# Performance work log

Hardware: AMD Instinct MI355X
Metric: run time of the kernel (lower is better)

## Reference

```python
import jax, jax.numpy as jnp
import numpy as np

Nc, Ns, Nt, d_h, BS = 64, 64, 64, 128, 16


def setup_inputs() -> dict:
    key = jax.random.key(0)
    k1, k2, k3, k4, k5 = jax.random.split(key, 5)
    Ac = (jax.random.uniform(k1, (Ns, Nc)) < 0.05).astype(jnp.float32)
    As = (jax.random.uniform(k2, (Ns, Ns)) < 0.05).astype(jnp.float32)
    # AA = As@As@Ac + As@Ac + Ac, then binarize (masked_fill(AA != 0, 1))
    AA = As @ As @ Ac + As @ Ac + Ac
    AA = (AA != 0).astype(jnp.float32)                 # [Ns, Nc]
    AA_mask = jnp.tile(AA, (Nt, Nt))                   # [Ns*Nt, Nc*Nt], == AA.repeat(Nt,Nt) in torch
    GCW = jax.random.normal(k3, (Ns * Nt, Nc * Nt), dtype=jnp.float32)
    GCB = jax.random.normal(k4, (Ns * Nt, d_h), dtype=jnp.float32)
    h = jax.random.normal(k5, (BS, Nc, Nt, d_h), dtype=jnp.float32)
    e = jnp.zeros((1,), jnp.float32)                   # unused in forward (kept for signature parity)
    return {"h": h, "e": e, "AA_mask": AA_mask, "GCW": GCW, "GCB": GCB}


def reference(h, e, AA_mask, GCW, GCB):
    bs = h.shape[0]
    # A = relu(AA.repeat(Nt,Nt) * GCW)  -- structured masked weight [Ns*Nt, Nc*Nt]
    A = jax.nn.relu(AA_mask * GCW)
    # h: [bs, Nc, Nt, d_h] -> [bs, Nt, Nc, d_h] -> [bs, Nt*Nc, d_h]
    x = jnp.transpose(h, (0, 2, 1, 3)).reshape(bs, Nt * Nc, d_h)
    # relu(A @ x + GCB): [bs, Ns*Nt, d_h]
    x = jax.nn.relu(jnp.einsum('ij,bjd->bid', A, x) + GCB)
    # [bs, Nt, Ns, d_h] -> [bs, Ns, Nt, d_h] (final torch reshape is a no-op)
    x = x.reshape(bs, Nt, Ns, d_h)
    x = jnp.transpose(x, (0, 2, 1, 3))
    return x
```

## Files before the change

kernel.cpp:

```cpp
#include <hip/hip_runtime.h>


#define NC 64
#define NS 64
#define NT 64
#define DH 128
#define BATCH 16
#define MDIM 4096
#define KDIM 4096
#define KPAD 4096
#define TM 128
#define TK 64
#define GBM 64
#define GBN 256
#define GBK 64

typedef __attribute__((ext_vector_type(8))) short short8;
typedef __attribute__((ext_vector_type(4))) short short4v;
typedef __attribute__((ext_vector_type(4))) float floatx4;

__device__ __forceinline__ unsigned short f2bf(float f) {
    union { float f; unsigned int i; } v; v.f = f;
    return (unsigned short)((v.i + 0x7fffu + ((v.i >> 16) & 1u)) >> 16);
}
__device__ __forceinline__ void async16(const void* g, void* l) {
    __builtin_amdgcn_global_load_lds(
        (const __attribute__((address_space(1))) void*)g,
        (__attribute__((address_space(3))) void*)l, 16, 0, 0);
}

__global__ __launch_bounds__(256)
void prep(const float* __restrict__ aam, const float* __restrict__ gcw,
          const float* __restrict__ hmat,
          unsigned short* __restrict__ Abf, unsigned short* __restrict__ XT,
          unsigned short* __restrict__ cidx, int* __restrict__ nsb)
{
    const int tid = threadIdx.x;
    if ((int)blockIdx.x < MDIM) {
        const int r  = blockIdx.x;
        const int s  = r >> 6;
        const int tt = r & 63;
        const int i  = tt * 64 + s;
        __shared__ unsigned short scidx[64];
        __shared__ int sns;
        __shared__ unsigned short srow[4096];
        if (tid < 64) {
            float v = aam[(size_t)s * KDIM + tid];
            unsigned long long m = __ballot(v != 0.f);
            int rank = __popcll(m & ((1ull << tid) - 1ull));
            if (v != 0.f) scidx[rank] = (unsigned short)tid;
            if (tid == 0) sns = (int)__popcll(m);
            if (tt == 0) {
                if (v != 0.f) cidx[s * 64 + rank] = (unsigned short)tid;
                if (tid == 0) nsb[s] = (int)__popcll(m);
            }
        }
        const float* gr = gcw + (size_t)i * KDIM;
#pragma unroll
        for (int u = 0; u < 4; ++u) {
            const int idx = u * 1024 + tid * 4;
            floatx4 wv = *(const floatx4*)(gr + idx);
            short4v p;
#pragma unroll
            for (int e = 0; e < 4; ++e) {
                float v = wv[e] > 0.f ? wv[e] : 0.f;
                p[e] = (short)f2bf(v);
            }
            *(short4v*)&srow[idx] = p;
        }
        __syncthreads();
        const int ke = sns * 64;
        for (int kk0 = tid * 8; kk0 < ke; kk0 += 2048) {
            const int c  = (int)scidx[kk0 >> 6];
            const int t0 = kk0 & 63;
            short8 p;
#pragma unroll
            for (int e = 0; e < 8; ++e)
                p[e] = (short)srow[(t0 + e) * 64 + c];
            *(short8*)(Abf + (size_t)r * KPAD + kk0) = p;
        }
    } else {
        const int blk = blockIdx.x - MDIM;
        const int b = blk >> 6;
        const int c = blk & 63;
        __shared__ unsigned short sx[64][136];
        const float* hp = hmat + (((size_t)b * NC + c) * NT) * DH;
#pragma unroll
        for (int u = 0; u < 8; ++u) {
            const int idx = u * 1024 + tid * 4;
            const int t = idx >> 7;
            const int d = idx & 127;
            floatx4 v = *(const floatx4*)(hp + idx);
            short4v p;
#pragma unroll
            for (int e = 0; e < 4; ++e) p[e] = (short)f2bf(v[e]);
            *(short4v*)&sx[t][d] = p;
        }
        __syncthreads();
        const int d  = tid >> 1;
        const int th = (tid & 1) * 32;
        unsigned short* dst = XT + ((size_t)(b * DH + d)) * KPAD + c * 64 + th;
#pragma unroll
        for (int u2 = 0; u2 < 4; ++u2) {
            short8 p;
#pragma unroll
            for (int e = 0; e < 8; ++e)
                p[e] = (short)sx[th + u2 * 8 + e][d];
            *(short8*)(dst + u2 * 8) = p;
        }
    }
}

__global__ __launch_bounds__(256, 2)
void gemm(const unsigned short* __restrict__ Abf,
          const unsigned short* __restrict__ XT,
          const unsigned short* __restrict__ cidx,
          const int* __restrict__ nsb,
          const float* __restrict__ gcb,
          float* __restrict__ out)
{
    __shared__ short lds[2][(GBM + GBN) * GBK];

    const int tid = threadIdx.x;
    const int bid = blockIdx.x;
    const int np = bid & 7;
    const int s  = bid >> 3;
    const int n0 = np * GBN;

    const int lane = tid & 63;
    const int w    = tid >> 6;
    const int wn   = w * 64;
    const int l15  = lane & 15;
    const int q    = lane >> 4;
    const int srow = lane >> 3;
    const int swz  = ((lane & 7) ^ srow) << 3;

    const int nt = nsb[s];
    const int cl = (int)cidx[s * 64 + lane];

    const unsigned short* Ab = Abf + (size_t)(s * 64) * KPAD + swz;
    const unsigned short* Xb = XT  + (size_t)n0 * KPAD + swz;

    floatx4 acc[4][4];
#pragma unroll
    for (int mi = 0; mi < 4; ++mi)
#pragma unroll
        for (int ni = 0; ni < 4; ++ni)
            acc[mi][ni] = (floatx4){0.f, 0.f, 0.f, 0.f};

    auto stage = [&](int t, int b) {
        short* dst = lds[b];
        const int c = __shfl(cl, t);
        const size_t ka = (size_t)t * GBK;
        const size_t kx = (size_t)c * GBK;
        async16(Ab + (size_t)(w * 8 + srow) * KPAD + ka,       dst + (w * 8) * GBK);
        async16(Ab + (size_t)((w + 4) * 8 + srow) * KPAD + ka, dst + ((w + 4) * 8) * GBK);
#pragma unroll
        for (int g = 0; g < 8; ++g) {
            const int rr = w * 64 + g * 8;
            async16(Xb + (size_t)(rr + srow) * KPAD + kx, dst + (GBM + rr) * GBK);
        }
    };

    auto compute = [&](int b) {
        const short* sA = lds[b];
        const short* sX = lds[b] + GBM * GBK;
#pragma unroll
        for (int h2 = 0; h2 < 2; ++h2) {
            const int co = ((h2 * 4 + q) ^ (l15 & 7)) << 3;
            short8 af[4], xf[4];
#pragma unroll
            for (int mi = 0; mi < 4; ++mi)
                af[mi] = *(const short8*)&sA[(mi * 16 + l15) * GBK + co];
#pragma unroll
            for (int ni = 0; ni < 4; ++ni)
                xf[ni] = *(const short8*)&sX[(wn + ni * 16 + l15) * GBK + co];
            __builtin_amdgcn_s_setprio(1);
#pragma unroll
            for (int mi = 0; mi < 4; ++mi)
#pragma unroll
                for (int ni = 0; ni < 4; ++ni)
                    acc[mi][ni] = __builtin_amdgcn_mfma_f32_16x16x32_bf16(
                        af[mi], xf[ni], acc[mi][ni], 0, 0, 0);
            __builtin_amdgcn_s_setprio(0);
        }
    };

    if (nt > 0) stage(0, 0);
    if (nt > 1) stage(1, 1);
    for (int t = 0; t < nt - 1; ++t) {
        asm volatile("s_waitcnt vmcnt(10)" ::: "memory");
        __builtin_amdgcn_s_barrier();
        compute(t & 1);
        __builtin_amdgcn_s_barrier();
        if (t + 2 < nt) stage(t + 2, t & 1);
    }
    if (nt > 0) {
        asm volatile("s_waitcnt vmcnt(0)" ::: "memory");
        __builtin_amdgcn_s_barrier();
        compute((nt - 1) & 1);
    }

#pragma unroll
    for (int mi = 0; mi < 4; ++mi) {
        const int tt0 = mi * 16 + q * 4;
#pragma unroll
        for (int ni = 0; ni < 4; ++ni) {
            const int n  = n0 + wn + ni * 16 + l15;
            const int bb = n >> 7;
            const int d  = n & 127;
#pragma unroll
            for (int r = 0; r < 4; ++r) {
                const int tt = tt0 + r;
                const int i  = tt * 64 + s;
                float v = acc[mi][ni][r] + gcb[(size_t)i * DH + d];
                v = v > 0.f ? v : 0.f;
                out[(((size_t)bb * NS + s) * NT + tt) * DH + d] = v;
            }
        }
    }
}

#define APAD 40
#define XPAD 20
__global__ __launch_bounds__(256, 2)
void gcn_fused(const float* __restrict__ hmat, const float* __restrict__ aam,
               const float* __restrict__ gcw, const float* __restrict__ gcb,
               float* __restrict__ out)
{
    __shared__ short sA[TM * APAD];
    __shared__ unsigned int sX[DH * XPAD];
    const int tid = threadIdx.x;
    const int bid = blockIdx.x;
    const int mp  = (bid & 7) * 4 + (bid >> 7);
    const int b   = (bid >> 3) & 15;
    const int i0  = mp * TM;
    const int lane = tid & 63;
    const int wm = ((tid >> 6) >> 1) * 64;
    const int wn = ((tid >> 6) & 1) * 64;
    const int l15 = lane & 15;
    const int q   = lane >> 4;
    floatx4 acc[4][4];
#pragma unroll
    for (int mi = 0; mi < 4; ++mi)
#pragma unroll
        for (int ni = 0; ni < 4; ++ni) acc[mi][ni] = (floatx4){0.f,0.f,0.f,0.f};
    const int ar = tid >> 2, ac = (tid & 3) << 3;
    const int kp = tid >> 4, dg = (tid & 15) << 3;
    const int wkey = (tid & 3) << 2;
    for (int k0 = 0; k0 < KDIM; k0 += 32) {
        const size_t ga0 = (size_t)(i0 + ar) * KDIM + (k0 + ac);
        const size_t ga1 = ga0 + (size_t)64 * KDIM;
        floatx4 aa0a = *(const floatx4*)(aam + ga0), aa0b = *(const floatx4*)(aam + ga0 + 4);
        floatx4 ww0a = *(const floatx4*)(gcw + ga0), ww0b = *(const floatx4*)(gcw + ga0 + 4);
        floatx4 aa1a = *(const floatx4*)(aam + ga1), aa1b = *(const floatx4*)(aam + ga1 + 4);
        floatx4 ww1a = *(const floatx4*)(gcw + ga1), ww1b = *(const floatx4*)(gcw + ga1 + 4);
        const int jj = k0 + 2 * kp, tt = jj >> 6, cc = jj & 63;
        const size_t gx0 = ((size_t)(b * NC + cc) * NT + tt) * DH + dg;
        const size_t gx1 = gx0 + (size_t)NT * DH;
        floatx4 x0a = *(const floatx4*)(hmat + gx0), x0b = *(const floatx4*)(hmat + gx0 + 4);
        floatx4 x1a = *(const floatx4*)(hmat + gx1), x1b = *(const floatx4*)(hmat + gx1 + 4);
        __syncthreads();
        short8 p0, p1;
#pragma unroll
        for (int e = 0; e < 4; ++e) {
            float v0 = aa0a[e]*ww0a[e]; v0 = v0>0.f?v0:0.f;
            float v1 = aa0b[e]*ww0b[e]; v1 = v1>0.f?v1:0.f;
            float v2 = aa1a[e]*ww1a[e]; v2 = v2>0.f?v2:0.f;
            float v3 = aa1b[e]*ww1b[e]; v3 = v3>0.f?v3:0.f;
            p0[e] = (short)f2bf(v0); p0[e+4] = (short)f2bf(v1);
            p1[e] = (short)f2bf(v2); p1[e+4] = (short)f2bf(v3);
        }
        *(short8*)&sA[ar * APAD + ac] = p0;
        *(short8*)&sA[(ar + 64) * APAD + ac] = p1;
#pragma unroll
        for (int e = 0; e < 4; ++e) {
            unsigned int pka = (unsigned int)f2bf(x0a[e]) | ((unsigned int)f2bf(x1a[e]) << 16);
            unsigned int pkb = (unsigned int)f2bf(x0b[e]) | ((unsigned int)f2bf(x1b[e]) << 16);
            sX[(dg + e) * XPAD + (kp ^ wkey)] = pka;
            sX[(dg + e + 4) * XPAD + (kp ^ wkey)] = pkb;
        }
        __syncthreads();
        short8 afrag[4], bfrag[4];
#pragma unroll
        for (int mi = 0; mi < 4; ++mi)
            afrag[mi] = *(const short8*)&sA[(wm + mi * 16 + l15) * APAD + q * 8];
#pragma unroll
        for (int ni = 0; ni < 4; ++ni) {
            const int row = wn + ni * 16 + l15;
            const int col = (q * 4) ^ (((row >> 3) & 3) << 2);
            bfrag[ni] = *(const short8*)(sX + row * XPAD + col);
        }
#pragma unroll
        for (int mi = 0; mi < 4; ++mi)
#pragma unroll
            for (int ni = 0; ni < 4; ++ni)
                acc[mi][ni] = __builtin_amdgcn_mfma_f32_16x16x32_bf16(
                    afrag[mi], bfrag[ni], acc[mi][ni], 0, 0, 0);
    }
#pragma unroll
    for (int mi = 0; mi < 4; ++mi) {
        const int ibase = i0 + wm + mi * 16 + q * 4;
#pragma unroll
        for (int ni = 0; ni < 4; ++ni) {
            const int d = wn + ni * 16 + l15;
#pragma unroll
            for (int r = 0; r < 4; ++r) {
                const int i = ibase + r;
                float v = acc[mi][ni][r] + gcb[(size_t)i * DH + d];
                v = v > 0.f ? v : 0.f;
                out[(((size_t)b * NS + (i & 63)) * NT + (i >> 6)) * DH + d] = v;
            }
        }
    }
}

extern "C" void kernel_launch(void* const* d_in, const int* in_sizes, int n_in,
                              void* d_out, int out_size, void* d_ws, size_t ws_size,
                              hipStream_t stream) {
    const float* h   = (const float*)d_in[0];
    const float* aam = (const float*)d_in[2];
    const float* gcw = (const float*)d_in[3];
    const float* gcb = (const float*)d_in[4];
    float* out = (float*)d_out;

    const size_t A_BYTES   = (size_t)MDIM * KPAD * 2;
    const size_t XT_BYTES  = (size_t)BATCH * DH * KPAD * 2;
    const size_t IDX_BYTES = 64 * 64 * 2;
    const size_t NS_BYTES  = 64 * 4;

    if (ws_size >= A_BYTES + XT_BYTES + IDX_BYTES + NS_BYTES) {
        unsigned short* Abf = (unsigned short*)d_ws;
        unsigned short* XTp = (unsigned short*)((char*)d_ws + A_BYTES);
        unsigned short* cid = (unsigned short*)((char*)d_ws + A_BYTES + XT_BYTES);
        int* nsb            = (int*)((char*)d_ws + A_BYTES + XT_BYTES + IDX_BYTES);
        prep<<<dim3(MDIM + BATCH * NT), 256, 0, stream>>>(aam, gcw, h, Abf, XTp, cid, nsb);
        gemm<<<dim3(64 * 8), 256, 0, stream>>>(Abf, XTp, cid, nsb, gcb, out);
    } else {
        gcn_fused<<<dim3((MDIM / TM) * BATCH), 256, 0, stream>>>(h, aam, gcw, gcb, out);
    }
}
```

Baseline: 229.3 us.

## Shrink GEMM N-tile to one batch, use 8 waves, and gather GCW directly

The GEMM tile shrinks from 256 to 128 columns, so each block covers a single batch. Blocks now have 512 threads in a 2x4 wave grid with 2x2 MFMA tiles per wave, and the grid doubles to 1024 blocks, which should raise occupancy and parallelism on the many CUs. The prep kernel no longer stages the whole GCW row through LDS; it reads only the needed sparse columns directly from global memory, cutting the loaded bytes to the nonzero blocks. The cost is strided, uncoalesced gathers in prep and less data reuse per block in the GEMM.

```diff
diff --git a/kernel.cpp b/kernel.cpp
--- a/kernel.cpp
+++ b/kernel.cpp
@@ -12,7 +12,7 @@
 #define TM 128
 #define TK 64
 #define GBM 64
-#define GBN 256
+#define GBN 128
 #define GBK 64
 
 typedef __attribute__((ext_vector_type(8))) short short8;
@@ -43,7 +43,6 @@
         const int i  = tt * 64 + s;
         __shared__ unsigned short scidx[64];
         __shared__ int sns;
-        __shared__ unsigned short srow[4096];
         if (tid < 64) {
             float v = aam[(size_t)s * KDIM + tid];
             unsigned long long m = __ballot(v != 0.f);
@@ -55,28 +54,19 @@
                 if (tid == 0) nsb[s] = (int)__popcll(m);
             }
         }
-        const float* gr = gcw + (size_t)i * KDIM;
-#pragma unroll
-        for (int u = 0; u < 4; ++u) {
-            const int idx = u * 1024 + tid * 4;
-            floatx4 wv = *(const floatx4*)(gr + idx);
-            short4v p;
-#pragma unroll
-            for (int e = 0; e < 4; ++e) {
-                float v = wv[e] > 0.f ? wv[e] : 0.f;
-                p[e] = (short)f2bf(v);
-            }
-            *(short4v*)&srow[idx] = p;
-        }
         __syncthreads();
         const int ke = sns * 64;
+        const float* gr = gcw + (size_t)i * KDIM;
         for (int kk0 = tid * 8; kk0 < ke; kk0 += 2048) {
             const int c  = (int)scidx[kk0 >> 6];
             const int t0 = kk0 & 63;
             short8 p;
 #pragma unroll
-            for (int e = 0; e < 8; ++e)
-                p[e] = (short)srow[(t0 + e) * 64 + c];
+            for (int e = 0; e < 8; ++e) {
+                float v = gr[(t0 + e) * 64 + c];
+                v = v > 0.f ? v : 0.f;
+                p[e] = (short)f2bf(v);
+            }
             *(short8*)(Abf + (size_t)r * KPAD + kk0) = p;
         }
     } else {
@@ -111,7 +101,7 @@
     }
 }
 
-__global__ __launch_bounds__(256, 2)
+__global__ __launch_bounds__(512, 6)
 void gemm(const unsigned short* __restrict__ Abf,
           const unsigned short* __restrict__ XT,
           const unsigned short* __restrict__ cidx,
@@ -123,13 +113,14 @@
 
     const int tid = threadIdx.x;
     const int bid = blockIdx.x;
-    const int np = bid & 7;
-    const int s  = bid >> 3;
+    const int np = bid & 15;
+    const int s  = bid >> 4;
     const int n0 = np * GBN;
 
     const int lane = tid & 63;
     const int w    = tid >> 6;
-    const int wn   = w * 64;
+    const int wm   = (w >> 2) * 32;
+    const int wn   = (w & 3) * 32;
     const int l15  = lane & 15;
     const int q    = lane >> 4;
     const int srow = lane >> 3;
@@ -141,11 +132,11 @@
     const unsigned short* Ab = Abf + (size_t)(s * 64) * KPAD + swz;
     const unsigned short* Xb = XT  + (size_t)n0 * KPAD + swz;
 
-    floatx4 acc[4][4];
-#pragma unroll
-    for (int mi = 0; mi < 4; ++mi)
-#pragma unroll
-        for (int ni = 0; ni < 4; ++ni)
+    floatx4 acc[2][2];
+#pragma unroll
+    for (int mi = 0; mi < 2; ++mi)
+#pragma unroll
+        for (int ni = 0; ni < 2; ++ni)
             acc[mi][ni] = (floatx4){0.f, 0.f, 0.f, 0.f};
 
     auto stage = [&](int t, int b) {
@@ -154,12 +145,8 @@
         const size_t ka = (size_t)t * GBK;
         const size_t kx = (size_t)c * GBK;
         async16(Ab + (size_t)(w * 8 + srow) * KPAD + ka,       dst + (w * 8) * GBK);
-        async16(Ab + (size_t)((w + 4) * 8 + srow) * KPAD + ka, dst + ((w + 4) * 8) * GBK);
-#pragma unroll
-        for (int g = 0; g < 8; ++g) {
-            const int rr = w * 64 + g * 8;
-            async16(Xb + (size_t)(rr + srow) * KPAD + kx, dst + (GBM + rr) * GBK);
-        }
+        async16(Xb + (size_t)(w * 8 + srow) * KPAD + kx,       dst + (GBM + w * 8) * GBK);
+        async16(Xb + (size_t)(64 + w * 8 + srow) * KPAD + kx,  dst + (GBM + 64 + w * 8) * GBK);
     };
 
     auto compute = [&](int b) {
@@ -168,18 +155,18 @@
 #pragma unroll
         for (int h2 = 0; h2 < 2; ++h2) {
             const int co = ((h2 * 4 + q) ^ (l15 & 7)) << 3;
-            short8 af[4], xf[4];
-#pragma unroll
-            for (int mi = 0; mi < 4; ++mi)
-                af[mi] = *(const short8*)&sA[(mi * 16 + l15) * GBK + co];
-#pragma unroll
-            for (int ni = 0; ni < 4; ++ni)
+            short8 af[2], xf[2];
+#pragma unroll
+            for (int mi = 0; mi < 2; ++mi)
+                af[mi] = *(const short8*)&sA[(wm + mi * 16 + l15) * GBK + co];
+#pragma unroll
+            for (int ni = 0; ni < 2; ++ni)
                 xf[ni] = *(const short8*)&sX[(wn + ni * 16 + l15) * GBK + co];
             __builtin_amdgcn_s_setprio(1);
 #pragma unroll
-            for (int mi = 0; mi < 4; ++mi)
-#pragma unroll
-                for (int ni = 0; ni < 4; ++ni)
+            for (int mi = 0; mi < 2; ++mi)
+#pragma unroll
+                for (int ni = 0; ni < 2; ++ni)
                     acc[mi][ni] = __builtin_amdgcn_mfma_f32_16x16x32_bf16(
                         af[mi], xf[ni], acc[mi][ni], 0, 0, 0);
             __builtin_amdgcn_s_setprio(0);
@@ -189,7 +176,7 @@
     if (nt > 0) stage(0, 0);
     if (nt > 1) stage(1, 1);
     for (int t = 0; t < nt - 1; ++t) {
-        asm volatile("s_waitcnt vmcnt(10)" ::: "memory");
+        asm volatile("s_waitcnt vmcnt(3)" ::: "memory");
         __builtin_amdgcn_s_barrier();
         compute(t & 1);
         __builtin_amdgcn_s_barrier();
@@ -202,20 +189,18 @@
     }
 
 #pragma unroll
-    for (int mi = 0; mi < 4; ++mi) {
-        const int tt0 = mi * 16 + q * 4;
-#pragma unroll
-        for (int ni = 0; ni < 4; ++ni) {
-            const int n  = n0 + wn + ni * 16 + l15;
-            const int bb = n >> 7;
-            const int d  = n & 127;
+    for (int mi = 0; mi < 2; ++mi) {
+        const int tt0 = wm + mi * 16 + q * 4;
+#pragma unroll
+        for (int ni = 0; ni < 2; ++ni) {
+            const int d = wn + ni * 16 + l15;
 #pragma unroll
             for (int r = 0; r < 4; ++r) {
                 const int tt = tt0 + r;
                 const int i  = tt * 64 + s;
                 float v = acc[mi][ni][r] + gcb[(size_t)i * DH + d];
                 v = v > 0.f ? v : 0.f;
-                out[(((size_t)bb * NS + s) * NT + tt) * DH + d] = v;
+                out[(((size_t)np * NS + s) * NT + tt) * DH + d] = v;
             }
         }
     }
@@ -335,7 +320,7 @@
         unsigned short* cid = (unsigned short*)((char*)d_ws + A_BYTES + XT_BYTES);
         int* nsb            = (int*)((char*)d_ws + A_BYTES + XT_BYTES + IDX_BYTES);
         prep<<<dim3(MDIM + BATCH * NT), 256, 0, stream>>>(aam, gcw, h, Abf, XTp, cid, nsb);
-        gemm<<<dim3(64 * 8), 256, 0, stream>>>(Abf, XTp, cid, nsb, gcb, out);
+        gemm<<<dim3(64 * 16), 512, 0, stream>>>(Abf, XTp, cid, nsb, gcb, out);
     } else {
         gcn_fused<<<dim3((MDIM / TM) * BATCH), 256, 0, stream>>>(h, aam, gcw, gcb, out);
     }
```

Result: no change. 233.5 us (+1.8%).

## Pair sparse row-blocks in GEMM to share X tiles and gather A directly

Applied to the files above, without the earlier changes.

The GEMM now handles two output row-blocks per workgroup. It uses 512 threads and an M tile of 128, and walks the union of their nonzero column-blocks. Each staged X tile is reused by both halves, and a wave's MFMA work is skipped when its half lacks that column-block. The prep kernel no longer stages full fp32 GCW rows through LDS. Each block handles four rows and gathers only the needed nonzero columns straight from global memory, and it builds the paired column index table. This trades fewer and larger GEMM blocks plus strided, uncoalesced global reads in prep for less X traffic and less wasted conversion work.

```diff
diff --git a/kernel.cpp b/kernel.cpp
--- a/kernel.cpp
+++ b/kernel.cpp
@@ -11,7 +11,7 @@
 #define KPAD 4096
 #define TM 128
 #define TK 64
-#define GBM 64
+#define GBM 128
 #define GBN 256
 #define GBK 64
 
@@ -33,54 +33,60 @@
 void prep(const float* __restrict__ aam, const float* __restrict__ gcw,
           const float* __restrict__ hmat,
           unsigned short* __restrict__ Abf, unsigned short* __restrict__ XT,
-          unsigned short* __restrict__ cidx, int* __restrict__ nsb)
+          int* __restrict__ cpair, int* __restrict__ ntp)
 {
     const int tid = threadIdx.x;
-    if ((int)blockIdx.x < MDIM) {
-        const int r  = blockIdx.x;
-        const int s  = r >> 6;
-        const int tt = r & 63;
-        const int i  = tt * 64 + s;
+    if ((int)blockIdx.x < 1024) {
+        const int blk = blockIdx.x;
+        const int s   = blk >> 4;
+        const int tt0 = (blk & 15) * 4;
         __shared__ unsigned short scidx[64];
         __shared__ int sns;
-        __shared__ unsigned short srow[4096];
         if (tid < 64) {
             float v = aam[(size_t)s * KDIM + tid];
             unsigned long long m = __ballot(v != 0.f);
             int rank = __popcll(m & ((1ull << tid) - 1ull));
             if (v != 0.f) scidx[rank] = (unsigned short)tid;
             if (tid == 0) sns = (int)__popcll(m);
-            if (tt == 0) {
-                if (v != 0.f) cidx[s * 64 + rank] = (unsigned short)tid;
-                if (tid == 0) nsb[s] = (int)__popcll(m);
+            if (tt0 == 0 && (s & 1) == 0) {
+                float v1 = aam[(size_t)(s + 1) * KDIM + tid];
+                unsigned long long m1 = __ballot(v1 != 0.f);
+                unsigned long long mu = m | m1;
+                if ((mu >> tid) & 1ull) {
+                    int ur  = __popcll(mu & ((1ull << tid) - 1ull));
+                    int ci0 = __popcll(m  & ((1ull << tid) - 1ull));
+                    int ci1 = __popcll(m1 & ((1ull << tid) - 1ull));
+                    int f0  = (int)((m  >> tid) & 1ull);
+                    int f1  = (int)((m1 >> tid) & 1ull);
+                    cpair[(s >> 1) * 64 + ur] =
+                        tid | (f0 << 6) | (f1 << 7) | (ci0 << 8) | (ci1 << 14);
+                }
+                if (tid == 0) ntp[s >> 1] = (int)__popcll(mu);
             }
-        }
-        const float* gr = gcw + (size_t)i * KDIM;
-#pragma unroll
-        for (int u = 0; u < 4; ++u) {
-            const int idx = u * 1024 + tid * 4;
-            floatx4 wv = *(const floatx4*)(gr + idx);
-            short4v p;
-#pragma unroll
-            for (int e = 0; e < 4; ++e) {
-                float v = wv[e] > 0.f ? wv[e] : 0.f;
-                p[e] = (short)f2bf(v);
-            }
-            *(short4v*)&srow[idx] = p;
         }
         __syncthreads();
         const int ke = sns * 64;
-        for (int kk0 = tid * 8; kk0 < ke; kk0 += 2048) {
-            const int c  = (int)scidx[kk0 >> 6];
-            const int t0 = kk0 & 63;
-            short8 p;
-#pragma unroll
-            for (int e = 0; e < 8; ++e)
-                p[e] = (short)srow[(t0 + e) * 64 + c];
-            *(short8*)(Abf + (size_t)r * KPAD + kk0) = p;
+#pragma unroll
+        for (int rr = 0; rr < 4; ++rr) {
+            const int tt = tt0 + rr;
+            const int i  = tt * 64 + s;
+            const int r  = s * 64 + tt;
+            const float* gr = gcw + (size_t)i * KDIM;
+            for (int kk0 = tid * 8; kk0 < ke; kk0 += 2048) {
+                const int c  = (int)scidx[kk0 >> 6];
+                const int t0 = kk0 & 63;
+                short8 p;
+#pragma unroll
+                for (int e = 0; e < 8; ++e) {
+                    float v = gr[(t0 + e) * 64 + c];
+                    v = v > 0.f ? v : 0.f;
+                    p[e] = (short)f2bf(v);
+                }
+                *(short8*)(Abf + (size_t)r * KPAD + kk0) = p;
+            }
         }
     } else {
-        const int blk = blockIdx.x - MDIM;
+        const int blk = blockIdx.x - 1024;
         const int b = blk >> 6;
         const int c = blk & 63;
         __shared__ unsigned short sx[64][136];
@@ -111,11 +117,11 @@
     }
 }
 
-__global__ __launch_bounds__(256, 2)
+__global__ __launch_bounds__(512, 2)
 void gemm(const unsigned short* __restrict__ Abf,
           const unsigned short* __restrict__ XT,
-          const unsigned short* __restrict__ cidx,
-          const int* __restrict__ nsb,
+          const int* __restrict__ cpair,
+          const int* __restrict__ ntp,
           const float* __restrict__ gcb,
           float* __restrict__ out)
 {
@@ -124,22 +130,24 @@
     const int tid = threadIdx.x;
     const int bid = blockIdx.x;
     const int np = bid & 7;
-    const int s  = bid >> 3;
+    const int p  = bid >> 3;
     const int n0 = np * GBN;
 
     const int lane = tid & 63;
     const int w    = tid >> 6;
-    const int wn   = w * 64;
+    const int wm   = (w >> 2) * 64;
+    const int wn   = (w & 3) * 64;
     const int l15  = lane & 15;
     const int q    = lane >> 4;
     const int srow = lane >> 3;
     const int swz  = ((lane & 7) ^ srow) << 3;
-
-    const int nt = nsb[s];
-    const int cl = (int)cidx[s * 64 + lane];
-
-    const unsigned short* Ab = Abf + (size_t)(s * 64) * KPAD + swz;
-    const unsigned short* Xb = XT  + (size_t)n0 * KPAD + swz;
+    const int half = wm >> 6;
+
+    const int nt = ntp[p];
+    const int ep = cpair[p * 64 + lane];
+
+    const unsigned short* Abp = Abf + (size_t)(p * 128) * KPAD + swz;
+    const unsigned short* Xb  = XT  + (size_t)n0 * KPAD + swz;
 
     floatx4 acc[4][4];
 #pragma unroll
@@ -150,14 +158,15 @@
 
     auto stage = [&](int t, int b) {
         short* dst = lds[b];
-        const int c = __shfl(cl, t);
-        const size_t ka = (size_t)t * GBK;
-        const size_t kx = (size_t)c * GBK;
-        async16(Ab + (size_t)(w * 8 + srow) * KPAD + ka,       dst + (w * 8) * GBK);
-        async16(Ab + (size_t)((w + 4) * 8 + srow) * KPAD + ka, dst + ((w + 4) * 8) * GBK);
-#pragma unroll
-        for (int g = 0; g < 8; ++g) {
-            const int rr = w * 64 + g * 8;
+        const int e   = __shfl(ep, t);
+        const int kx  = (e & 63) << 6;
+        const int ka0 = ((e >> 8) & 63) << 6;
+        const int ka1 = ((e >> 14) & 63) << 6;
+        async16(Abp + (size_t)(w * 8 + srow) * KPAD + ka0,      dst + (w * 8) * GBK);
+        async16(Abp + (size_t)(64 + w * 8 + srow) * KPAD + ka1, dst + (64 + w * 8) * GBK);
+#pragma unroll
+        for (int g = 0; g < 4; ++g) {
+            const int rr = g * 64 + w * 8;
             async16(Xb + (size_t)(rr + srow) * KPAD + kx, dst + (GBM + rr) * GBK);
         }
     };
@@ -171,7 +180,7 @@
             short8 af[4], xf[4];
 #pragma unroll
             for (int mi = 0; mi < 4; ++mi)
-                af[mi] = *(const short8*)&sA[(mi * 16 + l15) * GBK + co];
+                af[mi] = *(const short8*)&sA[(wm + mi * 16 + l15) * GBK + co];
 #pragma unroll
             for (int ni = 0; ni < 4; ++ni)
                 xf[ni] = *(const short8*)&sX[(wn + ni * 16 + l15) * GBK + co];
@@ -189,18 +198,21 @@
     if (nt > 0) stage(0, 0);
     if (nt > 1) stage(1, 1);
     for (int t = 0; t < nt - 1; ++t) {
-        asm volatile("s_waitcnt vmcnt(10)" ::: "memory");
+        asm volatile("s_waitcnt vmcnt(6)" ::: "memory");
         __builtin_amdgcn_s_barrier();
-        compute(t & 1);
+        const int f = (__shfl(ep, t) >> (6 + half)) & 1;
+        if (f) compute(t & 1);
         __builtin_amdgcn_s_barrier();
         if (t + 2 < nt) stage(t + 2, t & 1);
     }
     if (nt > 0) {
         asm volatile("s_waitcnt vmcnt(0)" ::: "memory");
         __builtin_amdgcn_s_barrier();
-        compute((nt - 1) & 1);
-    }
-
+        const int f = (__shfl(ep, nt - 1) >> (6 + half)) & 1;
+        if (f) compute((nt - 1) & 1);
+    }
+
+    const int s = 2 * p + half;
 #pragma unroll
     for (int mi = 0; mi < 4; ++mi) {
         const int tt0 = mi * 16 + q * 4;
@@ -326,16 +338,16 @@
 
     const size_t A_BYTES   = (size_t)MDIM * KPAD * 2;
     const size_t XT_BYTES  = (size_t)BATCH * DH * KPAD * 2;
-    const size_t IDX_BYTES = 64 * 64 * 2;
-    const size_t NS_BYTES  = 64 * 4;
-
-    if (ws_size >= A_BYTES + XT_BYTES + IDX_BYTES + NS_BYTES) {
+    const size_t CP_BYTES  = 32 * 64 * 4;
+    const size_t NTP_BYTES = 32 * 4;
+
+    if (ws_size >= A_BYTES + XT_BYTES + CP_BYTES + NTP_BYTES) {
         unsigned short* Abf = (unsigned short*)d_ws;
         unsigned short* XTp = (unsigned short*)((char*)d_ws + A_BYTES);
-        unsigned short* cid = (unsigned short*)((char*)d_ws + A_BYTES + XT_BYTES);
-        int* nsb            = (int*)((char*)d_ws + A_BYTES + XT_BYTES + IDX_BYTES);
-        prep<<<dim3(MDIM + BATCH * NT), 256, 0, stream>>>(aam, gcw, h, Abf, XTp, cid, nsb);
-        gemm<<<dim3(64 * 8), 256, 0, stream>>>(Abf, XTp, cid, nsb, gcb, out);
+        int* cpair          = (int*)((char*)d_ws + A_BYTES + XT_BYTES);
+        int* ntp            = (int*)((char*)d_ws + A_BYTES + XT_BYTES + CP_BYTES);
+        prep<<<dim3(2048), 256, 0, stream>>>(aam, gcw, h, Abf, XTp, cpair, ntp);
+        gemm<<<dim3(32 * 8), 512, 0, stream>>>(Abf, XTp, cpair, ntp, gcb, out);
     } else {
         gcn_fused<<<dim3((MDIM / TM) * BATCH), 256, 0, stream>>>(h, aam, gcw, gcb, out);
     }
```

After: 241.3 us. 1.05x slower.

## Pre-pack A and X in MFMA fragment layout and drop LDS staging in GEMM

Applied to the files above, without the earlier changes.

The prep kernel now writes the masked, ReLU'd bf16 weights and the transposed activations directly in per-lane MFMA fragment order. It also gathers only the weight columns that belong to nonzero mask blocks instead of converting full rows through LDS. The GEMM kernel loads fragments straight from global memory into registers with a two-stage register double buffer, removing LDS, async copies and barriers. The cost is that waves and blocks now load the same A fragments redundantly. The strided gathers from the weight matrix may also coalesce poorly.

```diff
diff --git a/kernel.cpp b/kernel.cpp
--- a/kernel.cpp
+++ b/kernel.cpp
@@ -8,12 +8,8 @@
 #define BATCH 16
 #define MDIM 4096
 #define KDIM 4096
-#define KPAD 4096
 #define TM 128
 #define TK 64
-#define GBM 64
-#define GBN 256
-#define GBK 64
 
 typedef __attribute__((ext_vector_type(8))) short short8;
 typedef __attribute__((ext_vector_type(4))) short short4v;
@@ -23,67 +19,64 @@
     union { float f; unsigned int i; } v; v.f = f;
     return (unsigned short)((v.i + 0x7fffu + ((v.i >> 16) & 1u)) >> 16);
 }
-__device__ __forceinline__ void async16(const void* g, void* l) {
-    __builtin_amdgcn_global_load_lds(
-        (const __attribute__((address_space(1))) void*)g,
-        (__attribute__((address_space(3))) void*)l, 16, 0, 0);
-}
 
 __global__ __launch_bounds__(256)
 void prep(const float* __restrict__ aam, const float* __restrict__ gcw,
           const float* __restrict__ hmat,
-          unsigned short* __restrict__ Abf, unsigned short* __restrict__ XT,
+          unsigned short* __restrict__ AF, unsigned short* __restrict__ XF,
           unsigned short* __restrict__ cidx, int* __restrict__ nsb)
 {
     const int tid = threadIdx.x;
-    if ((int)blockIdx.x < MDIM) {
-        const int r  = blockIdx.x;
-        const int s  = r >> 6;
-        const int tt = r & 63;
-        const int i  = tt * 64 + s;
+    if ((int)blockIdx.x < 1024) {
+        const int blk = blockIdx.x;
+        const int s   = blk >> 4;
         __shared__ unsigned short scidx[64];
         __shared__ int sns;
-        __shared__ unsigned short srow[4096];
         if (tid < 64) {
             float v = aam[(size_t)s * KDIM + tid];
             unsigned long long m = __ballot(v != 0.f);
             int rank = __popcll(m & ((1ull << tid) - 1ull));
             if (v != 0.f) scidx[rank] = (unsigned short)tid;
             if (tid == 0) sns = (int)__popcll(m);
-            if (tt == 0) {
+            if ((blk & 15) == 0) {
                 if (v != 0.f) cidx[s * 64 + rank] = (unsigned short)tid;
                 if (tid == 0) nsb[s] = (int)__popcll(m);
             }
         }
-        const float* gr = gcw + (size_t)i * KDIM;
-#pragma unroll
-        for (int u = 0; u < 4; ++u) {
-            const int idx = u * 1024 + tid * 4;
-            floatx4 wv = *(const floatx4*)(gr + idx);
-            short4v p;
-#pragma unroll
-            for (int e = 0; e < 4; ++e) {
-                float v = wv[e] > 0.f ? wv[e] : 0.f;
-                p[e] = (short)f2bf(v);
-            }
-            *(short4v*)&srow[idx] = p;
-        }
         __syncthreads();
-        const int ke = sns * 64;
-        for (int kk0 = tid * 8; kk0 < ke; kk0 += 2048) {
-            const int c  = (int)scidx[kk0 >> 6];
-            const int t0 = kk0 & 63;
-            short8 p;
-#pragma unroll
-            for (int e = 0; e < 8; ++e)
-                p[e] = (short)srow[(t0 + e) * 64 + c];
-            *(short8*)(Abf + (size_t)r * KPAD + kk0) = p;
+        const int lane = tid & 63;
+        const int l15  = lane & 15;
+        const int q    = lane >> 4;
+#pragma unroll
+        for (int cii = 0; cii < 4; ++cii) {
+            const int ci = (blk & 15) + cii * 16;
+            if (ci >= sns) continue;
+            const int c = (int)scidx[ci];
+#pragma unroll
+            for (int k2 = 0; k2 < 2; ++k2) {
+                const int combo = (tid >> 6) * 2 + k2;
+                const int hh = combo >> 2;
+                const int mg = combo & 3;
+                const int tt = mg * 16 + l15;
+                const int i  = tt * 64 + s;
+                const float* gr = gcw + (size_t)i * KDIM;
+                short8 p;
+#pragma unroll
+                for (int e = 0; e < 8; ++e) {
+                    const int t = hh * 32 + q * 8 + e;
+                    float v = gr[t * 64 + c];
+                    v = v > 0.f ? v : 0.f;
+                    p[e] = (short)f2bf(v);
+                }
+                *(short8*)(AF + ((((size_t)(s * 64 + ci)) * 2 + hh) * 4 + mg) * 512
+                              + lane * 8) = p;
+            }
         }
     } else {
-        const int blk = blockIdx.x - MDIM;
+        const int blk = blockIdx.x - 1024;
         const int b = blk >> 6;
         const int c = blk & 63;
-        __shared__ unsigned short sx[64][136];
+        __shared__ unsigned short sx[64][140];
         const float* hp = hmat + (((size_t)b * NC + c) * NT) * DH;
 #pragma unroll
         for (int u = 0; u < 8; ++u) {
@@ -97,49 +90,45 @@
             *(short4v*)&sx[t][d] = p;
         }
         __syncthreads();
-        const int d  = tid >> 1;
-        const int th = (tid & 1) * 32;
-        unsigned short* dst = XT + ((size_t)(b * DH + d)) * KPAD + c * 64 + th;
+        const int lane = tid & 63;
+        const int l15  = lane & 15;
+        const int q    = lane >> 4;
 #pragma unroll
         for (int u2 = 0; u2 < 4; ++u2) {
+            const int combo = (tid >> 6) * 4 + u2;
+            const int h2 = combo >> 3;
+            const int gl = combo & 7;
             short8 p;
 #pragma unroll
             for (int e = 0; e < 8; ++e)
-                p[e] = (short)sx[th + u2 * 8 + e][d];
-            *(short8*)(dst + u2 * 8) = p;
-        }
-    }
-}
-
-__global__ __launch_bounds__(256, 2)
-void gemm(const unsigned short* __restrict__ Abf,
-          const unsigned short* __restrict__ XT,
+                p[e] = (short)sx[h2 * 32 + q * 8 + e][gl * 16 + l15];
+            *(short8*)(XF + (((size_t)(c * 2 + h2)) * 128 + b * 8 + gl) * 512
+                          + lane * 8) = p;
+        }
+    }
+}
+
+__global__ __launch_bounds__(256)
+void gemm(const unsigned short* __restrict__ AF,
+          const unsigned short* __restrict__ XF,
           const unsigned short* __restrict__ cidx,
           const int* __restrict__ nsb,
           const float* __restrict__ gcb,
           float* __restrict__ out)
 {
-    __shared__ short lds[2][(GBM + GBN) * GBK];
-
     const int tid = threadIdx.x;
     const int bid = blockIdx.x;
     const int np = bid & 7;
     const int s  = bid >> 3;
-    const int n0 = np * GBN;
-
-    const int lane = tid & 63;
-    const int w    = tid >> 6;
-    const int wn   = w * 64;
-    const int l15  = lane & 15;
-    const int q    = lane >> 4;
-    const int srow = lane >> 3;
-    const int swz  = ((lane & 7) ^ srow) << 3;
-
-    const int nt = nsb[s];
-    const int cl = (int)cidx[s * 64 + lane];
-
-    const unsigned short* Ab = Abf + (size_t)(s * 64) * KPAD + swz;
-    const unsigned short* Xb = XT  + (size_t)n0 * KPAD + swz;
+
+    const int lane  = tid & 63;
+    const int w     = tid >> 6;
+    const int gbase = np * 16 + w * 4;
+    const int l15   = lane & 15;
+    const int q     = lane >> 4;
+
+    const int nt  = nsb[s];
+    const int clv = (int)cidx[s * 64 + lane];
 
     floatx4 acc[4][4];
 #pragma unroll
@@ -148,57 +137,42 @@
         for (int ni = 0; ni < 4; ++ni)
             acc[mi][ni] = (floatx4){0.f, 0.f, 0.f, 0.f};
 
-    auto stage = [&](int t, int b) {
-        short* dst = lds[b];
-        const int c = __shfl(cl, t);
-        const size_t ka = (size_t)t * GBK;
-        const size_t kx = (size_t)c * GBK;
-        async16(Ab + (size_t)(w * 8 + srow) * KPAD + ka,       dst + (w * 8) * GBK);
-        async16(Ab + (size_t)((w + 4) * 8 + srow) * KPAD + ka, dst + ((w + 4) * 8) * GBK);
-#pragma unroll
-        for (int g = 0; g < 8; ++g) {
-            const int rr = w * 64 + g * 8;
-            async16(Xb + (size_t)(rr + srow) * KPAD + kx, dst + (GBM + rr) * GBK);
-        }
+    short8 a0[4], x0[4], a1[4], x1[4];
+
+    auto loadh = [&](short8 af[4], short8 xf[4], int ci, int c, int hh) {
+        const size_t ab = ((((size_t)(s * 64 + ci)) * 2 + hh) * 4) * 512 + lane * 8;
+#pragma unroll
+        for (int mi = 0; mi < 4; ++mi)
+            af[mi] = *(const short8*)(AF + ab + mi * 512);
+        const size_t xb = (((size_t)(c * 2 + hh)) * 128 + gbase) * 512 + lane * 8;
+#pragma unroll
+        for (int ni = 0; ni < 4; ++ni)
+            xf[ni] = *(const short8*)(XF + xb + ni * 512);
     };
-
-    auto compute = [&](int b) {
-        const short* sA = lds[b];
-        const short* sX = lds[b] + GBM * GBK;
-#pragma unroll
-        for (int h2 = 0; h2 < 2; ++h2) {
-            const int co = ((h2 * 4 + q) ^ (l15 & 7)) << 3;
-            short8 af[4], xf[4];
-#pragma unroll
-            for (int mi = 0; mi < 4; ++mi)
-                af[mi] = *(const short8*)&sA[(mi * 16 + l15) * GBK + co];
+    auto mfmaset = [&](short8 af[4], short8 xf[4]) {
+#pragma unroll
+        for (int mi = 0; mi < 4; ++mi)
 #pragma unroll
             for (int ni = 0; ni < 4; ++ni)
-                xf[ni] = *(const short8*)&sX[(wn + ni * 16 + l15) * GBK + co];
-            __builtin_amdgcn_s_setprio(1);
-#pragma unroll
-            for (int mi = 0; mi < 4; ++mi)
-#pragma unroll
-                for (int ni = 0; ni < 4; ++ni)
-                    acc[mi][ni] = __builtin_amdgcn_mfma_f32_16x16x32_bf16(
-                        af[mi], xf[ni], acc[mi][ni], 0, 0, 0);
-            __builtin_amdgcn_s_setprio(0);
-        }
+                acc[mi][ni] = __builtin_amdgcn_mfma_f32_16x16x32_bf16(
+                    af[mi], xf[ni], acc[mi][ni], 0, 0, 0);
     };
 
-    if (nt > 0) stage(0, 0);
-    if (nt > 1) stage(1, 1);
-    for (int t = 0; t < nt - 1; ++t) {
-        asm volatile("s_waitcnt vmcnt(10)" ::: "memory");
-        __builtin_amdgcn_s_barrier();
-        compute(t & 1);
-        __builtin_amdgcn_s_barrier();
-        if (t + 2 < nt) stage(t + 2, t & 1);
-    }
     if (nt > 0) {
-        asm volatile("s_waitcnt vmcnt(0)" ::: "memory");
-        __builtin_amdgcn_s_barrier();
-        compute((nt - 1) & 1);
+        int ccur = __shfl(clv, 0);
+        loadh(a0, x0, 0, ccur, 0);
+        const int steps = nt * 2;
+        for (int k = 0; k + 1 < steps; k += 2) {
+            const int t = k >> 1;
+            loadh(a1, x1, t, ccur, 1);
+            mfmaset(a0, x0);
+            if (k + 2 < steps) {
+                const int cn = __shfl(clv, t + 1);
+                ccur = cn;
+                loadh(a0, x0, t + 1, cn, 0);
+            }
+            mfmaset(a1, x1);
+        }
     }
 
 #pragma unroll
@@ -206,7 +180,7 @@
         const int tt0 = mi * 16 + q * 4;
 #pragma unroll
         for (int ni = 0; ni < 4; ++ni) {
-            const int n  = n0 + wn + ni * 16 + l15;
+            const int n  = (gbase + ni) * 16 + l15;
             const int bb = n >> 7;
             const int d  = n & 127;
 #pragma unroll
@@ -324,18 +298,18 @@
     const float* gcb = (const float*)d_in[4];
     float* out = (float*)d_out;
 
-    const size_t A_BYTES   = (size_t)MDIM * KPAD * 2;
-    const size_t XT_BYTES  = (size_t)BATCH * DH * KPAD * 2;
+    const size_t A_BYTES   = (size_t)64 * 64 * 8 * 512 * 2;
+    const size_t X_BYTES   = (size_t)64 * 2 * 128 * 512 * 2;
     const size_t IDX_BYTES = 64 * 64 * 2;
     const size_t NS_BYTES  = 64 * 4;
 
-    if (ws_size >= A_BYTES + XT_BYTES + IDX_BYTES + NS_BYTES) {
-        unsigned short* Abf = (unsigned short*)d_ws;
-        unsigned short* XTp = (unsigned short*)((char*)d_ws + A_BYTES);
-        unsigned short* cid = (unsigned short*)((char*)d_ws + A_BYTES + XT_BYTES);
-        int* nsb            = (int*)((char*)d_ws + A_BYTES + XT_BYTES + IDX_BYTES);
-        prep<<<dim3(MDIM + BATCH * NT), 256, 0, stream>>>(aam, gcw, h, Abf, XTp, cid, nsb);
-        gemm<<<dim3(64 * 8), 256, 0, stream>>>(Abf, XTp, cid, nsb, gcb, out);
+    if (ws_size >= A_BYTES + X_BYTES + IDX_BYTES + NS_BYTES) {
+        unsigned short* AF = (unsigned short*)d_ws;
+        unsigned short* XF = (unsigned short*)((char*)d_ws + A_BYTES);
+        unsigned short* ci = (unsigned short*)((char*)d_ws + A_BYTES + X_BYTES);
+        int* nsb           = (int*)((char*)d_ws + A_BYTES + X_BYTES + IDX_BYTES);
+        prep<<<dim3(2048), 256, 0, stream>>>(aam, gcw, h, AF, XF, ci, nsb);
+        gemm<<<dim3(64 * 8), 256, 0, stream>>>(AF, XF, ci, nsb, gcb, out);
     } else {
         gcn_fused<<<dim3((MDIM / TM) * BATCH), 256, 0, stream>>>(h, aam, gcw, gcb, out);
     }
```

Measured after the change: 371.6 us. 62.1% more time.
